# Kernel optimization log

Measured on AMD Instinct MI355X. Metric: run time of the kernel, lower is better.

Reference implementation:

```python
import jax, jax.numpy as jnp
import numpy as np

B, L, D_MODEL = 4, 4096, 1024
D_STATE = 16
DT_RANK = D_MODEL // 16  # 64
K = 4  # conv kernel size
EPS = 1e-5


def setup_inputs() -> dict:
    key = jax.random.key(0)
    ks = jax.random.split(key, 8)
    s = 0.02
    f = jax.random.normal(ks[0], (B, L, D_MODEL), dtype=jnp.float32)
    ln_g = jnp.ones((D_MODEL,), jnp.float32)
    ln_b = jnp.zeros((D_MODEL,), jnp.float32)
    Wx = jax.random.normal(ks[1], (D_MODEL, D_MODEL), jnp.float32) * s
    bx = jnp.zeros((D_MODEL,), jnp.float32)
    conv_w = jax.random.normal(ks[2], (D_MODEL, K), jnp.float32) * 0.1
    conv_b = jax.random.normal(ks[3], (D_MODEL,), jnp.float32) * s
    Wxp = jax.random.normal(ks[4], (D_MODEL, DT_RANK + 2 * D_STATE), jnp.float32) * s
    Wdt = jax.random.normal(ks[5], (DT_RANK, D_MODEL), jnp.float32) * s
    # negative bias keeps delta small so the (non-exponentiated) recurrence
    # h = (delta*A)*h + ... stays stable over L=4096 steps (|delta*A| < 1)
    bdt = jnp.full((D_MODEL,), -4.0, jnp.float32)
    A_log = jnp.tile(jnp.log(jnp.arange(1, D_STATE + 1, dtype=jnp.float32)), (D_MODEL, 1))
    Dp = jnp.ones((D_MODEL,), jnp.float32)
    return {"f": f, "ln_g": ln_g, "ln_b": ln_b, "Wx": Wx, "bx": bx,
            "conv_w": conv_w, "conv_b": conv_b, "Wxp": Wxp, "Wdt": Wdt,
            "bdt": bdt, "A_log": A_log, "Dp": Dp}


def reference(f, ln_g, ln_b, Wx, bx, conv_w, conv_b, Wxp, Wdt, bdt, A_log, Dp):
    b, l, d = f.shape
    # LayerNorm
    mu = jnp.mean(f, axis=-1, keepdims=True)
    var = jnp.mean(jnp.square(f - mu), axis=-1, keepdims=True)
    fn = (f - mu) * jax.lax.rsqrt(var + EPS) * ln_g + ln_b
    # input projection
    x = fn @ Wx + bx  # (b, l, d)
    # depthwise causal conv1d (torch pad=3 both sides then truncate to l == left-pad 3)
    xp = jnp.pad(x, ((0, 0), (K - 1, 0), (0, 0)))
    windows = jnp.stack([xp[:, k:k + l, :] for k in range(K)], axis=-1)  # (b, l, d, k)
    x = jnp.einsum('bldk,dk->bld', windows, conv_w) + conv_b
    x = jax.nn.silu(x)
    # selective SSM
    x_dbl = x @ Wxp  # (b, l, dt_rank + 2*n)
    dt = x_dbl[..., :DT_RANK]
    Bm = x_dbl[..., DT_RANK:DT_RANK + D_STATE]
    Cm = x_dbl[..., DT_RANK + D_STATE:]
    delta = jax.nn.softplus(dt @ Wdt + bdt)  # (b, l, d)
    A = -jnp.exp(A_log)  # (d, n)

    def step(h, inp):
        d_t, B_t, C_t, x_t = inp  # (b,d) (b,n) (b,n) (b,d)
        dA = d_t[:, :, None] * A                                  # (b, d, n)
        dB = (d_t * x_t)[:, :, None] * B_t[:, None, :]            # (b, d, n)
        h = dA * h + dB
        y = jnp.einsum('bdn,bn->bd', h, C_t)
        return h, y

    h0 = jnp.zeros((b, d, D_STATE), x.dtype)
    xs = (jnp.swapaxes(delta, 0, 1), jnp.swapaxes(Bm, 0, 1),
          jnp.swapaxes(Cm, 0, 1), jnp.swapaxes(x, 0, 1))
    _, ys = jax.lax.scan(step, h0, xs)  # ys: (l, b, d)
    y = jnp.swapaxes(ys, 0, 1) + x * Dp
    return y
```

## Files before the change

### kernel.cpp

```cpp
#include <hip/hip_runtime.h>
#include <cstdint>
#include <cstddef>

#define D_MODEL 1024
#define SEQ_L   4096
#define BATCH   4
#define NROWS   (BATCH*SEQ_L)
#define DSTATE  16
#define DTRANK  64
#define NDBL    96
#define CLEN    64
#define WARM    16
#define CT      16

typedef __attribute__((ext_vector_type(8))) _Float16 f16x8;
typedef __attribute__((ext_vector_type(4))) _Float16 h4;
typedef __attribute__((ext_vector_type(8))) _Float16 h8;
typedef __attribute__((ext_vector_type(4))) float f32x4;
typedef __attribute__((ext_vector_type(2))) float f32x2;

__device__ __forceinline__ float silu(float v) {
  return v / (1.f + __expf(-v));
}

__device__ __forceinline__ float softplus(float z) {
  return (z > 20.f) ? z : __logf(1.f + __expf(z));
}

__device__ __forceinline__ int swz64(int r, int e) { return e ^ ((r & 7) << 3); }

__global__ __launch_bounds__(256) void ln_kernel(const float* __restrict__ f,
                                                 const float* __restrict__ g,
                                                 const float* __restrict__ bta,
                                                 _Float16* __restrict__ fnb) {
  int row = blockIdx.x;
  int tid = threadIdx.x;
  const float* fr = f + (size_t)row * D_MODEL;
  float4 v = *(const float4*)&fr[tid * 4];
  float s  = v.x + v.y + v.z + v.w;
  float ss = v.x*v.x + v.y*v.y + v.z*v.z + v.w*v.w;
  #pragma unroll
  for (int o = 32; o > 0; o >>= 1) { s += __shfl_down(s, o); ss += __shfl_down(ss, o); }
  __shared__ float rs[8];
  int lane = tid & 63, w = tid >> 6;
  if (lane == 0) { rs[w] = s; rs[4 + w] = ss; }
  __syncthreads();
  if (tid == 0) {
    float S = rs[0] + rs[1] + rs[2] + rs[3];
    float SS = rs[4] + rs[5] + rs[6] + rs[7];
    float mu = S * (1.f / D_MODEL);
    float var = SS * (1.f / D_MODEL) - mu * mu;
    rs[0] = mu; rs[1] = rsqrtf(var + 1e-5f);
  }
  __syncthreads();
  float mu = rs[0], rstd = rs[1];
  float4 gv = *(const float4*)&g[tid * 4];
  float4 bv = *(const float4*)&bta[tid * 4];
  h4 o;
  o.x = (_Float16)((v.x - mu) * rstd * gv.x + bv.x);
  o.y = (_Float16)((v.y - mu) * rstd * gv.y + bv.y);
  o.z = (_Float16)((v.z - mu) * rstd * gv.z + bv.z);
  o.w = (_Float16)((v.w - mu) * rstd * gv.w + bv.w);
  *(h4*)&fnb[(size_t)row * D_MODEL + tid * 4] = o;
}

__global__ __launch_bounds__(256) void tcast(const float* __restrict__ W,
                                             _Float16* __restrict__ Wt,
                                             int rows, int cols) {
  __shared__ float tile[32][33];
  int tx = threadIdx.x & 31, ty = threadIdx.x >> 5;
  int c0 = blockIdx.x * 32, r0 = blockIdx.y * 32;
  #pragma unroll
  for (int i = 0; i < 4; ++i) {
    int r = ty + i * 8;
    tile[r][tx] = W[(size_t)(r0 + r) * cols + c0 + tx];
  }
  __syncthreads();
  #pragma unroll
  for (int i = 0; i < 4; ++i) {
    int n = ty + i * 8;
    Wt[(size_t)(c0 + n) * rows + r0 + tx] = (_Float16)tile[tx][n];
  }
}

__global__ __launch_bounds__(256, 4) void gemm1(const _Float16* __restrict__ Ab,
                                                const _Float16* __restrict__ Bt,
                                                const float* __restrict__ bias,
                                                _Float16* __restrict__ C) {
  __shared__ __align__(16) _Float16 As[128 * 64];
  __shared__ __align__(16) _Float16 Bs[128 * 64];
  const int K = D_MODEL, N = D_MODEL;
  int tid = threadIdx.x;
  int row0 = blockIdx.x * 128;
  int col0 = blockIdx.y * 128;
  int wave = tid >> 6, lane = tid & 63;
  int wr = wave >> 1, wc = wave & 1;
  int lr = lane & 15, half = lane >> 4;
  f32x4 acc[4][4] = {};

  int r_[4], gofs[4], wofs[4];
  #pragma unroll
  for (int i = 0; i < 4; ++i) {
    int c = tid + i * 256;
    int r = c >> 3, kc = c & 7;
    r_[i] = r;
    gofs[i] = kc * 8;
    wofs[i] = r * 64 + ((kc ^ (r & 7)) * 8);
  }

  for (int ks = 0; ks < 16; ++ks) {
    int k0 = ks * 64;
    h8 av[4], bv[4];
    #pragma unroll
    for (int i = 0; i < 4; ++i) {
      av[i] = *(const h8*)&Ab[(size_t)(row0 + r_[i]) * K + k0 + gofs[i]];
      bv[i] = *(const h8*)&Bt[(size_t)(col0 + r_[i]) * K + k0 + gofs[i]];
    }
    __syncthreads();
    #pragma unroll
    for (int i = 0; i < 4; ++i) {
      *(h8*)&As[wofs[i]] = av[i];
      *(h8*)&Bs[wofs[i]] = bv[i];
    }
    __syncthreads();
    #pragma unroll
    for (int kk = 0; kk < 2; ++kk) {
      int kch = ((kk * 4 + half) ^ (lr & 7)) * 8;
      f16x8 a[4], b[4];
      #pragma unroll
      for (int m = 0; m < 4; ++m)
        a[m] = *(const f16x8*)&As[(wr * 64 + m * 16 + lr) * 64 + kch];
      #pragma unroll
      for (int n = 0; n < 4; ++n)
        b[n] = *(const f16x8*)&Bs[(wc * 64 + n * 16 + lr) * 64 + kch];
      #pragma unroll
      for (int m = 0; m < 4; ++m)
        #pragma unroll
        for (int n = 0; n < 4; ++n)
          acc[m][n] = __builtin_amdgcn_mfma_f32_16x16x32_f16(b[n], a[m], acc[m][n], 0, 0, 0);
    }
  }
  #pragma unroll
  for (int m = 0; m < 4; ++m) {
    int gr = row0 + wr * 64 + m * 16 + lr;
    #pragma unroll
    for (int n = 0; n < 4; ++n) {
      int gc = col0 + wc * 64 + n * 16 + half * 4;
      float4 bv = *(const float4*)&bias[gc];
      h4 o;
      o.x = (_Float16)(acc[m][n][0] + bv.x);
      o.y = (_Float16)(acc[m][n][1] + bv.y);
      o.z = (_Float16)(acc[m][n][2] + bv.z);
      o.w = (_Float16)(acc[m][n][3] + bv.w);
      *(h4*)&C[(size_t)gr * N + gc] = o;
    }
  }
}

__global__ __launch_bounds__(256) void conv_silu(const _Float16* __restrict__ xlin,
                                                 const float* __restrict__ cw,
                                                 const float* __restrict__ cb,
                                                 _Float16* __restrict__ xo) {
  int idx = blockIdx.x * 256 + threadIdx.x;
  int d8 = idx & 127;
  int tg = idx >> 7;
  int row0 = tg * CT;
  int l0 = row0 & (SEQ_L - 1);
  int d = d8 * 8;
  float w[8][4];
  #pragma unroll
  for (int j = 0; j < 8; ++j) {
    float4 t = *(const float4*)&cw[(d + j) * 4];
    w[j][0] = t.x; w[j][1] = t.y; w[j][2] = t.z; w[j][3] = t.w;
  }
  float bias[8];
  #pragma unroll
  for (int j = 0; j < 8; j += 4) {
    float4 cbv = *(const float4*)&cb[d + j];
    bias[j] = cbv.x; bias[j+1] = cbv.y; bias[j+2] = cbv.z; bias[j+3] = cbv.w;
  }
  float win0[8], win1[8], win2[8];
  if (l0 == 0) {
    #pragma unroll
    for (int j = 0; j < 8; ++j) { win0[j] = 0.f; win1[j] = 0.f; win2[j] = 0.f; }
  } else {
    h8 m3 = *(const h8*)&xlin[(size_t)(row0 - 3) * D_MODEL + d];
    h8 m2 = *(const h8*)&xlin[(size_t)(row0 - 2) * D_MODEL + d];
    h8 m1 = *(const h8*)&xlin[(size_t)(row0 - 1) * D_MODEL + d];
    #pragma unroll
    for (int j = 0; j < 8; ++j) { win0[j] = (float)m3[j]; win1[j] = (float)m2[j]; win2[j] = (float)m1[j]; }
  }
  #pragma unroll
  for (int tt = 0; tt < CT; tt += 4) {
    h8 ld[4];
    #pragma unroll
    for (int k = 0; k < 4; ++k)
      ld[k] = *(const h8*)&xlin[(size_t)(row0 + tt + k) * D_MODEL + d];
    #pragma unroll
    for (int k = 0; k < 4; ++k) {
      float cur[8];
      #pragma unroll
      for (int j = 0; j < 8; ++j) cur[j] = (float)ld[k][j];
      h8 o;
      #pragma unroll
      for (int j = 0; j < 8; ++j) {
        float v = bias[j] + win0[j]*w[j][0] + win1[j]*w[j][1] + win2[j]*w[j][2] + cur[j]*w[j][3];
        o[j] = (_Float16)silu(v);
      }
      *(h8*)&xo[(size_t)(row0 + tt + k) * D_MODEL + d] = o;
      #pragma unroll
      for (int j = 0; j < 8; ++j) { win0[j] = win1[j]; win1[j] = win2[j]; win2[j] = cur[j]; }
    }
  }
}

__global__ __launch_bounds__(256) void gemm2(const _Float16* __restrict__ X,
                                             const _Float16* __restrict__ WT,
                                             float* __restrict__ Y) {
  __shared__ __align__(16) _Float16 As[64 * 64];
  __shared__ __align__(16) _Float16 Bs[96 * 64];
  int tid = threadIdx.x;
  int row0 = blockIdx.x * 64;
  int wave = tid >> 6, lane = tid & 63;
  int lr = lane & 15, half = lane >> 4;
  f32x4 acc[6] = {};
  for (int k0 = 0; k0 < D_MODEL; k0 += 64) {
    __syncthreads();
    #pragma unroll
    for (int i = 0; i < 2; ++i) {
      int cc = tid + i * 256;
      int r = cc >> 3, ko = (cc & 7) * 8;
      *(h8*)&As[r * 64 + swz64(r, ko)] = *(const h8*)&X[(size_t)(row0 + r) * D_MODEL + k0 + ko];
    }
    #pragma unroll
    for (int i = 0; i < 3; ++i) {
      int cc = tid + i * 256;
      int r = cc >> 3, ko = (cc & 7) * 8;
      *(h8*)&Bs[r * 64 + swz64(r, ko)] = *(const h8*)&WT[(size_t)r * D_MODEL + k0 + ko];
    }
    __syncthreads();
    #pragma unroll
    for (int kk = 0; kk < 2; ++kk) {
      f16x8 a = *(const f16x8*)&As[(wave * 16 + lr) * 64 + swz64(lr, kk * 32 + half * 8)];
      #pragma unroll
      for (int n = 0; n < 6; ++n) {
        f16x8 b = *(const f16x8*)&Bs[(n * 16 + lr) * 64 + swz64(lr, kk * 32 + half * 8)];
        acc[n] = __builtin_amdgcn_mfma_f32_16x16x32_f16(b, a, acc[n], 0, 0, 0);
      }
    }
  }
  int gr = row0 + wave * 16 + lr;
  #pragma unroll
  for (int n = 0; n < 6; ++n) {
    int gc = n * 16 + half * 4;
    *(f32x4*)&Y[(size_t)gr * NDBL + gc] = acc[n];
  }
}

__global__ __launch_bounds__(256) void gemm3(const float* __restrict__ XD,
                                             const _Float16* __restrict__ WT,
                                             const float* __restrict__ bdt,
                                             _Float16* __restrict__ Dl) {
  __shared__ __align__(16) _Float16 As[128 * 64];
  __shared__ __align__(16) _Float16 Bs[128 * 64];
  int tid = threadIdx.x;
  int row0 = blockIdx.x * 128;
  int col0 = blockIdx.y * 128;
  int wave = tid >> 6, lane = tid & 63;
  int wr = wave >> 1, wc = wave & 1;
  int lr = lane & 15, half = lane >> 4;
  #pragma unroll
  for (int i = 0; i < 8; ++i) {
    int cc = tid + i * 256;
    int r = cc >> 4, ko = (cc & 15) * 4;
    float4 v = *(const float4*)&XD[(size_t)(row0 + r) * NDBL + ko];
    h4 o; o.x = (_Float16)v.x; o.y = (_Float16)v.y; o.z = (_Float16)v.z; o.w = (_Float16)v.w;
    *(h4*)&As[r * 64 + swz64(r, ko)] = o;
  }
  #pragma unroll
  for (int i = 0; i < 4; ++i) {
    int cc = tid + i * 256;
    int r = cc >> 3, ko = (cc & 7) * 8;
    *(h8*)&Bs[r * 64 + swz64(r, ko)] = *(const h8*)&WT[(size_t)(col0 + r) * DTRANK + ko];
  }
  __syncthreads();
  f32x4 acc[4][4] = {};
  #pragma unroll
  for (int kk = 0; kk < 2; ++kk) {
    f16x8 a[4], b[4];
    #pragma unroll
    for (int m = 0; m < 4; ++m)
      a[m] = *(const f16x8*)&As[(wr * 64 + m * 16 + lr) * 64 + swz64(lr, kk * 32 + half * 8)];
    #pragma unroll
    for (int n = 0; n < 4; ++n)
      b[n] = *(const f16x8*)&Bs[(wc * 64 + n * 16 + lr) * 64 + swz64(lr, kk * 32 + half * 8)];
    #pragma unroll
    for (int m = 0; m < 4; ++m)
      #pragma unroll
      for (int n = 0; n < 4; ++n)
        acc[m][n] = __builtin_amdgcn_mfma_f32_16x16x32_f16(b[n], a[m], acc[m][n], 0, 0, 0);
  }
  #pragma unroll
  for (int m = 0; m < 4; ++m) {
    int gr = row0 + wr * 64 + m * 16 + lr;
    #pragma unroll
    for (int n = 0; n < 4; ++n) {
      int gc = col0 + wc * 64 + n * 16 + half * 4;
      float4 bv = *(const float4*)&bdt[gc];
      h4 o;
      o.x = (_Float16)softplus(acc[m][n][0] + bv.x);
      o.y = (_Float16)softplus(acc[m][n][1] + bv.y);
      o.z = (_Float16)softplus(acc[m][n][2] + bv.z);
      o.w = (_Float16)softplus(acc[m][n][3] + bv.w);
      *(h4*)&Dl[(size_t)gr * D_MODEL + gc] = o;
    }
  }
}

__global__ __launch_bounds__(256) void scan(const _Float16* __restrict__ delta,
                                            const _Float16* __restrict__ x,
                                            const float* __restrict__ xdbl,
                                            const float* __restrict__ A_log,
                                            const float* __restrict__ Dp,
                                            float* __restrict__ out) {
  int c = blockIdx.x, b = blockIdx.y, dq = blockIdx.z;
  int tid = threadIdx.x;
  int d = dq * 256 + tid;
  int warm = (c == 0) ? 0 : WARM;
  int t0 = c * CLEN - warm;
  int nt = CLEN + warm;
  __shared__ __align__(16) float Bl[(CLEN + WARM) * 16];
  __shared__ __align__(16) float Cl[(CLEN + WARM) * 16];
  int rowbase = b * SEQ_L + t0;
  for (int i = tid; i < nt * 4; i += 256) {
    int t = i >> 2, no = (i & 3) * 4;
    *(float4*)&Bl[t * 16 + no] = *(const float4*)&xdbl[(size_t)(rowbase + t) * NDBL + DTRANK + no];
    *(float4*)&Cl[t * 16 + no] = *(const float4*)&xdbl[(size_t)(rowbase + t) * NDBL + DTRANK + DSTATE + no];
  }
  __syncthreads();
  f32x2 Ar2[8], h2[8];
  #pragma unroll
  for (int q = 0; q < 4; ++q) {
    float4 al = *(const float4*)&A_log[d * 16 + q * 4];
    Ar2[q*2+0] = (f32x2){-__expf(al.x), -__expf(al.y)};
    Ar2[q*2+1] = (f32x2){-__expf(al.z), -__expf(al.w)};
  }
  #pragma unroll
  for (int q = 0; q < 8; ++q) h2[q] = (f32x2){0.f, 0.f};
  float dpv = Dp[d];
  const _Float16* dp_ = delta + (size_t)rowbase * D_MODEL + d;
  const _Float16* xp_ = x + (size_t)rowbase * D_MODEL + d;
  float* op_ = out + (size_t)rowbase * D_MODEL + d;
  const int PF = 8;
  float dnx[PF], xnx[PF];
  #pragma unroll
  for (int k = 0; k < PF; ++k) {
    dnx[k] = (float)dp_[(size_t)k * D_MODEL];
    xnx[k] = (float)xp_[(size_t)k * D_MODEL];
  }
  for (int tb = 0; tb < nt; tb += PF) {
    float dcur[PF], xcur[PF];
    #pragma unroll
    for (int k = 0; k < PF; ++k) { dcur[k] = dnx[k]; xcur[k] = xnx[k]; }
    if (tb + PF < nt) {
      #pragma unroll
      for (int k = 0; k < PF; ++k) {
        dnx[k] = (float)dp_[(size_t)(tb + PF + k) * D_MODEL];
        xnx[k] = (float)xp_[(size_t)(tb + PF + k) * D_MODEL];
      }
    }
    #pragma unroll
    for (int k = 0; k < PF; ++k) {
      int t = tb + k;
      float dlt = dcur[k], xv = xcur[k];
      float dx = dlt * xv;
      f32x2 dlt2 = (f32x2){dlt, dlt};
      f32x2 dx2  = (f32x2){dx, dx};
      f32x2 y2   = (f32x2){0.f, 0.f};
      const float4* Bp = (const float4*)&Bl[t * 16];
      const float4* Cp = (const float4*)&Cl[t * 16];
      #pragma unroll
      for (int q = 0; q < 4; ++q) {
        float4 bq = Bp[q];
        float4 cq = Cp[q];
        f32x2 blo = (f32x2){bq.x, bq.y}, bhi = (f32x2){bq.z, bq.w};
        f32x2 clo = (f32x2){cq.x, cq.y}, chi = (f32x2){cq.z, cq.w};
        f32x2 alo = dlt2 * Ar2[q*2+0];
        f32x2 ahi = dlt2 * Ar2[q*2+1];
        h2[q*2+0] = alo * h2[q*2+0] + dx2 * blo;
        h2[q*2+1] = ahi * h2[q*2+1] + dx2 * bhi;
        y2 = y2 + h2[q*2+0] * clo;
        y2 = y2 + h2[q*2+1] * chi;
      }
      if (t >= warm)
        __builtin_nontemporal_store(y2[0] + y2[1] + xv * dpv, &op_[(size_t)t * D_MODEL]);
    }
  }
}

extern "C" void kernel_launch(void* const* d_in, const int* in_sizes, int n_in,
                              void* d_out, int out_size, void* d_ws, size_t ws_size,
                              hipStream_t stream) {
  const float* f     = (const float*)d_in[0];
  const float* ln_g  = (const float*)d_in[1];
  const float* ln_b  = (const float*)d_in[2];
  const float* Wx    = (const float*)d_in[3];
  const float* bx    = (const float*)d_in[4];
  const float* convw = (const float*)d_in[5];
  const float* convb = (const float*)d_in[6];
  const float* Wxp   = (const float*)d_in[7];
  const float* Wdt   = (const float*)d_in[8];
  const float* bdt   = (const float*)d_in[9];
  const float* A_log = (const float*)d_in[10];
  const float* Dp    = (const float*)d_in[11];
  float* out = (float*)d_out;
  char* ws = (char*)d_ws;

  _Float16* fnb  = (_Float16*)(ws);
  _Float16* xlin = (_Float16*)(ws + 33554432);
  _Float16* xbuf = (_Float16*)(ws + 67108864);
  float*    xdbl = (float*)(ws + 100663296);
  _Float16* wxt  = (_Float16*)(ws + 106954752);
  _Float16* wxpT = (_Float16*)(ws + 109051904);
  _Float16* wdtT = (_Float16*)(ws + 109248512);
  _Float16* delta = xlin;

  tcast<<<dim3(32, 32), dim3(256), 0, stream>>>(Wx, wxt, 1024, 1024);
  tcast<<<dim3(3, 32),  dim3(256), 0, stream>>>(Wxp, wxpT, 1024, 96);
  tcast<<<dim3(32, 2),  dim3(256), 0, stream>>>(Wdt, wdtT, 64, 1024);
  ln_kernel<<<dim3(NROWS), dim3(256), 0, stream>>>(f, ln_g, ln_b, fnb);
  gemm1<<<dim3(NROWS / 128, D_MODEL / 128), dim3(256), 0, stream>>>(fnb, wxt, bx, xlin);
  conv_silu<<<dim3((NROWS / CT) * (D_MODEL / 8) / 256), dim3(256), 0, stream>>>(xlin, convw, convb, xbuf);
  gemm2<<<dim3(NROWS / 64), dim3(256), 0, stream>>>(xbuf, wxpT, xdbl);
  gemm3<<<dim3(NROWS / 128, D_MODEL / 128), dim3(256), 0, stream>>>(xdbl, wdtT, bdt, delta);
  scan<<<dim3(SEQ_L / CLEN, BATCH, 4), dim3(256), 0, stream>>>(delta, xbuf, xdbl, A_log, Dp, out);
}
```

Before: 163.5 us.

## Split scan state across two lanes per channel with shuffle reduction

The scan kernel now assigns each channel's 16 SSM states to two lanes, each holding 8 states, and combines the partial outputs with a cross-half shuffle. The grid doubles along the channel dimension to keep coverage the same. This halves per-thread register state and serial work per step, which should raise occupancy and parallelism. The cost is duplicated delta/x loads in both halves, an extra shuffle per timestep, and only half the lanes doing stores. A bias variable in the GEMM epilogue is also renamed.

```diff
diff --git a/kernel.cpp b/kernel.cpp
--- a/kernel.cpp
+++ b/kernel.cpp
@@ -146,12 +146,12 @@
     #pragma unroll
     for (int n = 0; n < 4; ++n) {
       int gc = col0 + wc * 64 + n * 16 + half * 4;
-      float4 bv = *(const float4*)&bias[gc];
+      float4 bv4 = *(const float4*)&bias[gc];
       h4 o;
-      o.x = (_Float16)(acc[m][n][0] + bv.x);
-      o.y = (_Float16)(acc[m][n][1] + bv.y);
-      o.z = (_Float16)(acc[m][n][2] + bv.z);
-      o.w = (_Float16)(acc[m][n][3] + bv.w);
+      o.x = (_Float16)(acc[m][n][0] + bv4.x);
+      o.y = (_Float16)(acc[m][n][1] + bv4.y);
+      o.z = (_Float16)(acc[m][n][2] + bv4.z);
+      o.w = (_Float16)(acc[m][n][3] + bv4.w);
       *(h4*)&C[(size_t)gr * N + gc] = o;
     }
   }
@@ -325,7 +325,10 @@
                                             float* __restrict__ out) {
   int c = blockIdx.x, b = blockIdx.y, dq = blockIdx.z;
   int tid = threadIdx.x;
-  int d = dq * 256 + tid;
+  int l = tid & 63, w = tid >> 6;
+  int sh = l >> 5;
+  int ch = w * 32 + (l & 31);
+  int d = dq * 128 + ch;
   int warm = (c == 0) ? 0 : WARM;
   int t0 = c * CLEN - warm;
   int nt = CLEN + warm;
@@ -338,15 +341,17 @@
     *(float4*)&Cl[t * 16 + no] = *(const float4*)&xdbl[(size_t)(rowbase + t) * NDBL + DTRANK + DSTATE + no];
   }
   __syncthreads();
-  f32x2 Ar2[8], h2[8];
-  #pragma unroll
-  for (int q = 0; q < 4; ++q) {
-    float4 al = *(const float4*)&A_log[d * 16 + q * 4];
-    Ar2[q*2+0] = (f32x2){-__expf(al.x), -__expf(al.y)};
-    Ar2[q*2+1] = (f32x2){-__expf(al.z), -__expf(al.w)};
-  }
-  #pragma unroll
-  for (int q = 0; q < 8; ++q) h2[q] = (f32x2){0.f, 0.f};
+  f32x2 Ar2[4], h2[4];
+  {
+    float4 a0 = *(const float4*)&A_log[d * 16 + sh * 8];
+    float4 a1 = *(const float4*)&A_log[d * 16 + sh * 8 + 4];
+    Ar2[0] = (f32x2){-__expf(a0.x), -__expf(a0.y)};
+    Ar2[1] = (f32x2){-__expf(a0.z), -__expf(a0.w)};
+    Ar2[2] = (f32x2){-__expf(a1.x), -__expf(a1.y)};
+    Ar2[3] = (f32x2){-__expf(a1.z), -__expf(a1.w)};
+  }
+  #pragma unroll
+  for (int q = 0; q < 4; ++q) h2[q] = (f32x2){0.f, 0.f};
   float dpv = Dp[d];
   const _Float16* dp_ = delta + (size_t)rowbase * D_MODEL + d;
   const _Float16* xp_ = x + (size_t)rowbase * D_MODEL + d;
@@ -377,23 +382,25 @@
       f32x2 dlt2 = (f32x2){dlt, dlt};
       f32x2 dx2  = (f32x2){dx, dx};
       f32x2 y2   = (f32x2){0.f, 0.f};
-      const float4* Bp = (const float4*)&Bl[t * 16];
-      const float4* Cp = (const float4*)&Cl[t * 16];
+      int base = t * 16 + sh * 8;
+      float4 b0 = *(const float4*)&Bl[base];
+      float4 b1 = *(const float4*)&Bl[base + 4];
+      float4 c0 = *(const float4*)&Cl[base];
+      float4 c1 = *(const float4*)&Cl[base + 4];
+      f32x2 bp[4] = {(f32x2){b0.x, b0.y}, (f32x2){b0.z, b0.w},
+                     (f32x2){b1.x, b1.y}, (f32x2){b1.z, b1.w}};
+      f32x2 cp[4] = {(f32x2){c0.x, c0.y}, (f32x2){c0.z, c0.w},
+                     (f32x2){c1.x, c1.y}, (f32x2){c1.z, c1.w}};
       #pragma unroll
       for (int q = 0; q < 4; ++q) {
-        float4 bq = Bp[q];
-        float4 cq = Cp[q];
-        f32x2 blo = (f32x2){bq.x, bq.y}, bhi = (f32x2){bq.z, bq.w};
-        f32x2 clo = (f32x2){cq.x, cq.y}, chi = (f32x2){cq.z, cq.w};
-        f32x2 alo = dlt2 * Ar2[q*2+0];
-        f32x2 ahi = dlt2 * Ar2[q*2+1];
-        h2[q*2+0] = alo * h2[q*2+0] + dx2 * blo;
-        h2[q*2+1] = ahi * h2[q*2+1] + dx2 * bhi;
-        y2 = y2 + h2[q*2+0] * clo;
-        y2 = y2 + h2[q*2+1] * chi;
+        f32x2 a = dlt2 * Ar2[q];
+        h2[q] = a * h2[q] + dx2 * bp[q];
+        y2 = y2 + h2[q] * cp[q];
       }
-      if (t >= warm)
-        __builtin_nontemporal_store(y2[0] + y2[1] + xv * dpv, &op_[(size_t)t * D_MODEL]);
+      float y = y2[0] + y2[1];
+      y += __shfl_xor(y, 32);
+      if (sh == 0 && t >= warm)
+        __builtin_nontemporal_store(y + xv * dpv, &op_[(size_t)t * D_MODEL]);
     }
   }
 }
@@ -433,5 +440,5 @@
   conv_silu<<<dim3((NROWS / CT) * (D_MODEL / 8) / 256), dim3(256), 0, stream>>>(xlin, convw, convb, xbuf);
   gemm2<<<dim3(NROWS / 64), dim3(256), 0, stream>>>(xbuf, wxpT, xdbl);
   gemm3<<<dim3(NROWS / 128, D_MODEL / 128), dim3(256), 0, stream>>>(xdbl, wdtT, bdt, delta);
-  scan<<<dim3(SEQ_L / CLEN, BATCH, 4), dim3(256), 0, stream>>>(delta, xbuf, xdbl, A_log, Dp, out);
-}
+  scan<<<dim3(SEQ_L / CLEN, BATCH, 8), dim3(256), 0, stream>>>(delta, xbuf, xdbl, A_log, Dp, out);
+}
```

Result: slower. 181.9 us (+11.2%).
